# Kernel optimization log

Hardware: AMD Instinct MI355X
Metric: run time of the kernel (lower is better)

## Reference

```python
import jax, jax.numpy as jnp
import numpy as np

DIM = 1024
N_HEADS = 16
HEAD_DIM = DIM // N_HEADS
B, S = 2, 2048
NEG = -1e9  # additive causal mask value (finite, safe in low precision)


def setup_inputs() -> dict:
    key = jax.random.key(0)
    k_x, k_q, k_k, k_v, k_o = jax.random.split(key, 5)
    x = jax.random.normal(k_x, (B, S, DIM), dtype=jnp.float32)
    # causal additive mask, broadcastable to [B, H, S, S]
    causal = jnp.triu(jnp.ones((S, S), dtype=bool), k=1)
    mask = jnp.where(causal, NEG, 0.0).astype(jnp.float32)[None, None]
    scale = 1.0 / np.sqrt(DIM)
    wq = jax.random.normal(k_q, (DIM, DIM), dtype=jnp.float32) * scale
    wk = jax.random.normal(k_k, (DIM, DIM), dtype=jnp.float32) * scale
    wv = jax.random.normal(k_v, (DIM, DIM), dtype=jnp.float32) * scale
    wo = jax.random.normal(k_o, (DIM, DIM), dtype=jnp.float32) * scale
    return {"x": x, "mask": mask, "wq": wq, "wk": wk, "wv": wv, "wo": wo}


def reference(x, mask, wq, wk, wv, wo):
    bs, seqlen, _ = x.shape
    # nn.Linear(y) = y @ W^T ; weights stored as (out, in)
    q = (x @ wq.T).reshape(bs, seqlen, N_HEADS, HEAD_DIM)
    k = (x @ wk.T).reshape(bs, seqlen, N_HEADS, HEAD_DIM)
    v = (x @ wv.T).reshape(bs, seqlen, N_HEADS, HEAD_DIM)
    # scores: [B, H, S, S] — intentionally materialized, as in the original
    attn = jnp.einsum('bqhd,bkhd->bhqk', q, k) / np.sqrt(HEAD_DIM)
    attn = attn + mask
    attn = jax.nn.softmax(attn, axis=-1)
    out = jnp.einsum('bhqk,bkhd->bqhd', attn, v).reshape(bs, seqlen, DIM)
    return out @ wo.T
```

## Files before the change

### kernel.cpp

```cpp
#include <hip/hip_runtime.h>

typedef __attribute__((ext_vector_type(8))) short bf16x8;
typedef __attribute__((ext_vector_type(4))) float f32x4;
typedef __attribute__((ext_vector_type(16))) float f32x16;
typedef __attribute__((ext_vector_type(4))) unsigned short u16x4;
typedef __attribute__((ext_vector_type(8))) unsigned short u16x8;

#define DIM 1024
#define SEQ 2048
#define NHEAD 16
#define HDIM 64
#define C2 0.18033688011112042f

#define WAIT_VM4() asm volatile("s_waitcnt vmcnt(4)" ::: "memory")
#define WAIT_VM0() asm volatile("s_waitcnt vmcnt(0)" ::: "memory")
#define BAR() __builtin_amdgcn_s_barrier()
#define SCHEDB() __builtin_amdgcn_sched_barrier(0)

__device__ __forceinline__ unsigned short f2bf(float f) {
  union { float f; unsigned u; } v; v.f = f;
  unsigned r = v.u + 0x7fffu + ((v.u >> 16) & 1u);
  return (unsigned short)(r >> 16);
}

__device__ __forceinline__ float bf2f(unsigned short s) {
  union { unsigned u; float f; } v; v.u = ((unsigned)s) << 16;
  return v.f;
}

__device__ __forceinline__ void gload_lds16(const void* g, void* l) {
  __builtin_amdgcn_global_load_lds(
      (const __attribute__((address_space(1))) void*)g,
      (__attribute__((address_space(3))) void*)l, 16, 0, 0);
}

__device__ __forceinline__ f32x16 mfma32(bf16x8 a, bf16x8 b, f32x16 c) {
  return __builtin_amdgcn_mfma_f32_32x32x16_bf16(a, b, c, 0, 0, 0);
}

__device__ __forceinline__ unsigned cvtpk(float lo, float hi) {
  unsigned r;
  asm("v_cvt_pk_bf16_f32 %0, %1, %2" : "=v"(r) : "v"(lo), "v"(hi));
  return r;
}

__global__ void f2bf_all(const float* __restrict__ x, const float* __restrict__ wq,
                         const float* __restrict__ wk, const float* __restrict__ wv,
                         const float* __restrict__ wo, unsigned short* __restrict__ xb,
                         unsigned short* __restrict__ wb) {
  int blk = blockIdx.x;
  const float* src;
  unsigned short* dst;
  int rb;
  if (blk < 4096) { src = x; dst = xb; rb = blk; }
  else {
    int w = (blk - 4096) >> 10;
    src = w == 0 ? wq : w == 1 ? wk : w == 2 ? wv : wo;
    dst = wb + (size_t)w * 1048576;
    rb = (blk - 4096) & 1023;
  }
  int i = rb * 256 + threadIdx.x;
  float4 v = ((const float4*)src)[i];
  u16x4 o;
  o[0] = f2bf(v.x); o[1] = f2bf(v.y); o[2] = f2bf(v.z); o[3] = f2bf(v.w);
  ((u16x4*)dst)[i] = o;
}

__global__ __launch_bounds__(256) void gemm3(
    const unsigned short* __restrict__ xb,
    const unsigned short* __restrict__ wb,
    unsigned short* __restrict__ qkv) {
  __shared__ unsigned short As[2][4096];
  __shared__ unsigned short Bs[2][4096];
  const int bz = blockIdx.x;
  const unsigned short *A, *B;
  unsigned short* C;
  int m0, n0, ldc;
  float cscale = 1.0f;
  if (bz < 512) {
    int xcd = bz & 7, inner = bz >> 3;
    int mm = inner & 3, n = (inner >> 2) & 7, w = inner >> 5;
    m0 = (xcd * 4 + mm) * 128; n0 = n * 128;
    A = xb; B = wb + w * 1048576; C = qkv + w * 4194304; ldc = 1024;
    if (w == 0) cscale = C2;
  } else {
    int idx = bz - 512;
    int xcd = idx & 7, inner = idx >> 3;
    int tt = inner & 3, mv = inner >> 2;
    m0 = mv * 128; n0 = (xcd * 4 + tt) * 128;
    A = wb + 2 * 1048576; B = xb; C = qkv + 2 * 4194304; ldc = 4096;
  }
  const int tid = threadIdx.x;
  const int wv = tid >> 6, lane = tid & 63;
  const int g = lane >> 4, l16 = lane & 15;
  const int wm = (wv >> 1) * 64, wn = (wv & 1) * 64;
  const int sro = lane >> 2, sc4 = lane & 3;
  f32x4 acc[4][4] = {};

#define GSTAGE(IT, BUF)                                                        \
  {                                                                            \
    const int kt = (IT) * 32;                                                  \
    _Pragma("unroll")                                                          \
    for (int s = 0; s < 2; ++s) {                                              \
      int r = wv * 32 + s * 16 + sro;                                          \
      int cd = sc4 ^ ((r >> 1) & 3);                                           \
      gload_lds16(A + (long long)(m0 + r) * 1024 + kt + cd * 8,                \
                  &As[BUF][wv * 1024 + s * 512]);                              \
      gload_lds16(B + (long long)(n0 + r) * 1024 + kt + cd * 8,                \
                  &Bs[BUF][wv * 1024 + s * 512]);                              \
    }                                                                          \
  }

  GSTAGE(0, 0);
  GSTAGE(1, 1);

  for (int it = 0; it < 32; ++it) {
    const int buf = it & 1;
    WAIT_VM4();
    BAR();
    SCHEDB();
    bf16x8 af[4], bfr[4];
#pragma unroll
    for (int mf = 0; mf < 4; ++mf) {
      int row = wm + mf * 16 + l16;
      af[mf] = *(const bf16x8*)((const char*)&As[buf][0] + row * 64 +
                                ((g ^ ((row >> 1) & 3)) << 4));
    }
#pragma unroll
    for (int nf = 0; nf < 4; ++nf) {
      int row = wn + nf * 16 + l16;
      bfr[nf] = *(const bf16x8*)((const char*)&Bs[buf][0] + row * 64 +
                                 ((g ^ ((row >> 1) & 3)) << 4));
    }
#pragma unroll
    for (int mf = 0; mf < 4; ++mf)
#pragma unroll
      for (int nf = 0; nf < 4; ++nf)
        acc[mf][nf] = __builtin_amdgcn_mfma_f32_16x16x32_bf16(
            af[mf], bfr[nf], acc[mf][nf], 0, 0, 0);
    SCHEDB();
    BAR();
    if (it + 1 < 32) {
      int nx = (it + 2 < 32) ? it + 2 : 31;
      GSTAGE(nx, buf);
    }
  }

#pragma unroll
  for (int mf = 0; mf < 4; ++mf)
#pragma unroll
    for (int nf = 0; nf < 4; ++nf)
#pragma unroll
      for (int r = 0; r < 4; ++r) {
        long long m = m0 + wm + mf * 16 + g * 4 + r;
        long long n = n0 + wn + nf * 16 + l16;
        C[m * ldc + n] = f2bf(acc[mf][nf][r] * cscale);
      }
}

__global__ __launch_bounds__(256) void gemm_out(
    const unsigned short* __restrict__ A,
    const unsigned short* __restrict__ B,
    float* __restrict__ C) {
  __shared__ unsigned short As[2][4096];
  __shared__ unsigned short Bs[2][4096];
  const int tid = threadIdx.x;
  const int wv = tid >> 6, lane = tid & 63;
  const int g = lane >> 4, l16 = lane & 15;
  const int m0 = blockIdx.y * 128, n0 = blockIdx.x * 128;
  const int wm = (wv >> 1) * 64, wn = (wv & 1) * 64;
  const int sro = lane >> 2, sc4 = lane & 3;
  f32x4 acc[4][4] = {};

#define OSTAGE(IT, BUF)                                                        \
  {                                                                            \
    const int kt = (IT) * 32;                                                  \
    _Pragma("unroll")                                                          \
    for (int s = 0; s < 2; ++s) {                                              \
      int r = wv * 32 + s * 16 + sro;                                          \
      int cd = sc4 ^ ((r >> 1) & 3);                                           \
      gload_lds16(A + (long long)(m0 + r) * 1024 + kt + cd * 8,                \
                  &As[BUF][wv * 1024 + s * 512]);                              \
      gload_lds16(B + (long long)(n0 + r) * 1024 + kt + cd * 8,                \
                  &Bs[BUF][wv * 1024 + s * 512]);                              \
    }                                                                          \
  }

  OSTAGE(0, 0);
  OSTAGE(1, 1);

  for (int it = 0; it < 32; ++it) {
    const int buf = it & 1;
    WAIT_VM4();
    BAR();
    SCHEDB();
    bf16x8 af[4], bfr[4];
#pragma unroll
    for (int mf = 0; mf < 4; ++mf) {
      int row = wm + mf * 16 + l16;
      af[mf] = *(const bf16x8*)((const char*)&As[buf][0] + row * 64 +
                                ((g ^ ((row >> 1) & 3)) << 4));
    }
#pragma unroll
    for (int nf = 0; nf < 4; ++nf) {
      int row = wn + nf * 16 + l16;
      bfr[nf] = *(const bf16x8*)((const char*)&Bs[buf][0] + row * 64 +
                                 ((g ^ ((row >> 1) & 3)) << 4));
    }
#pragma unroll
    for (int mf = 0; mf < 4; ++mf)
#pragma unroll
      for (int nf = 0; nf < 4; ++nf)
        acc[mf][nf] = __builtin_amdgcn_mfma_f32_16x16x32_bf16(
            af[mf], bfr[nf], acc[mf][nf], 0, 0, 0);
    SCHEDB();
    BAR();
    if (it + 1 < 32) {
      int nx = (it + 2 < 32) ? it + 2 : 31;
      OSTAGE(nx, buf);
    }
  }

#pragma unroll
  for (int mf = 0; mf < 4; ++mf)
#pragma unroll
    for (int nf = 0; nf < 4; ++nf)
#pragma unroll
      for (int r = 0; r < 4; ++r) {
        long long m = m0 + wm + mf * 16 + g * 4 + r;
        long long n = n0 + wn + nf * 16 + l16;
        C[m * 1024 + n] = acc[mf][nf][r];
      }
}

__global__ __launch_bounds__(256, 4) void attn_kernel(
    const unsigned short* __restrict__ Qg,
    const unsigned short* __restrict__ Kg,
    const unsigned short* __restrict__ VTg,
    unsigned short* __restrict__ Og,
    unsigned short* __restrict__ pacc,
    float* __restrict__ pml) {
  __shared__ unsigned short Kls[2][4096];
  __shared__ unsigned short Vls[2][4096];

  const int tid = threadIdx.x;
  const int wv = tid >> 6, lane = tid & 63;
  const int l32 = lane & 31, hi = lane >> 5;
  const int h = blockIdx.y, b = blockIdx.z;

  const int i = blockIdx.x;
  int qt, c, cn;
  if (i < 16)      { qt = 15 - (i >> 2); c = i & 3; cn = 4; }
  else if (i < 28) { int j = i - 16; qt = 11 - j / 3; c = j % 3; cn = 3; }
  else if (i < 36) { int j = i - 28; qt = 7 - ((j >> 1)); c = j & 1; cn = 2; }
  else             { qt = 39 - i; c = 0; cn = 1; }

  const int nt = 2 * qt + 2;
  const int t0 = c * 8;
  const int tb = min(t0 + 8, nt);
  const int umax = 4 * qt + wv;

  const int q = qt * 128 + wv * 32 + l32;
  const long long bh = (long long)b * SEQ * DIM + h * HDIM;
  const long long vbase = (long long)h * HDIM * 4096 + b * SEQ;

  const unsigned short* Qrow = Qg + (long long)(b * SEQ + q) * DIM + h * HDIM;
  bf16x8 qf[4];
#pragma unroll
  for (int ds = 0; ds < 4; ++ds)
    qf[ds] = *(const bf16x8*)(Qrow + ds * 16 + hi * 8);
  WAIT_VM0();

  bf16x8 ones;
#pragma unroll
  for (int j = 0; j < 8; ++j) ones[j] = (short)0x3F80;

  f32x16 acc0 = {}, acc1 = {}, lacc = {};

  const int sr = lane >> 3, sc = lane & 7;
#define STAGE(T, BUF)                                                          \
  {                                                                            \
    const int kv0s = (T) * 64;                                                 \
    _Pragma("unroll")                                                          \
    for (int s = 0; s < 2; ++s) {                                              \
      int jj = wv * 2 + s;                                                     \
      int r = jj * 8 + sr;                                                     \
      int cs = (sc ^ (r & 7)) * 8;                                             \
      gload_lds16(Kg + bh + (long long)(kv0s + r) * DIM + cs,                  \
                  &Kls[BUF][jj * 512]);                                        \
      gload_lds16(VTg + vbase + (long long)r * 4096 + kv0s + cs,               \
                  &Vls[BUF][jj * 512]);                                        \
    }                                                                          \
  }

  STAGE(t0, 0);
  { int nx = (t0 + 1 < tb) ? t0 + 1 : tb - 1; STAGE(nx, 1); }

  for (int t = t0; t < tb; ++t) {
    const int buf = (t - t0) & 1;
    WAIT_VM4();
    BAR();
    SCHEDB();

#pragma unroll
    for (int s = 0; s < 2; ++s) {
      const int u = 2 * t + s;
      if (u <= umax) {
        f32x16 sv = {};
        __builtin_amdgcn_s_setprio(1);
#pragma unroll
        for (int ds = 0; ds < 4; ++ds) {
          const int cbk = (((ds << 1) | hi) ^ (l32 & 7)) * 16;
          bf16x8 kf = *(const bf16x8*)((const char*)&Kls[buf][0] +
                                       (s * 32 + l32) * 128 + cbk);
          sv = mfma32(kf, qf[ds], sv);
        }
        __builtin_amdgcn_s_setprio(0);

        if (u == umax) {
#pragma unroll
          for (int r = 0; r < 16; ++r) {
            int kw = (r & 3) + 8 * (r >> 2) + 4 * hi;
            if (kw > l32) sv[r] = -1e30f;
          }
        }

#pragma unroll
        for (int r = 0; r < 16; ++r) sv[r] = exp2f(sv[r]);

        __builtin_amdgcn_s_setprio(1);
#pragma unroll
        for (int kk = 0; kk < 2; ++kk) {
          const int base = kk * 8;
          unsigned a0 = cvtpk(sv[base + 0], sv[base + 1]);
          unsigned a1 = cvtpk(sv[base + 2], sv[base + 3]);
          unsigned a2 = cvtpk(sv[base + 4], sv[base + 5]);
          unsigned a3 = cvtpk(sv[base + 6], sv[base + 7]);
          asm("v_permlane32_swap_b32 %0, %1" : "+v"(a0), "+v"(a2));
          asm("v_permlane32_swap_b32 %0, %1" : "+v"(a1), "+v"(a3));
          union { unsigned u4[4]; bf16x8 v; } pf;
          pf.u4[0] = a0; pf.u4[1] = a1; pf.u4[2] = a2; pf.u4[3] = a3;
          const int slice = 2 * s + kk;
          const int cbv = (((slice << 1) | hi) ^ (l32 & 7)) * 16;
          bf16x8 v0 = *(const bf16x8*)((const char*)&Vls[buf][0] + l32 * 128 + cbv);
          bf16x8 v1 = *(const bf16x8*)((const char*)&Vls[buf][0] + (32 + l32) * 128 + cbv);
          acc0 = mfma32(v0, pf.v, acc0);
          acc1 = mfma32(v1, pf.v, acc1);
          lacc = mfma32(ones, pf.v, lacc);
        }
        __builtin_amdgcn_s_setprio(0);
      }
    }
    SCHEDB();
    BAR();
    if (t + 1 < tb) {
      int nx = (t + 2 < tb) ? t + 2 : tb - 1;
      STAGE(nx, buf);
    }
  }

  const float l_run = lacc[0];

  if (cn == 1) {
    const float inv_l = 1.0f / l_run;
    unsigned short* Orow = Og + (long long)(b * SEQ + q) * DIM + h * HDIM;
#pragma unroll
    for (int dblk = 0; dblk < 2; ++dblk) {
#pragma unroll
      for (int g4 = 0; g4 < 4; ++g4) {
        u16x4 o;
#pragma unroll
        for (int jv = 0; jv < 4; ++jv) {
          float v = (dblk ? acc1[g4 * 4 + jv] : acc0[g4 * 4 + jv]) * inv_l;
          o[jv] = f2bf(v);
        }
        *(u16x4*)(Orow + dblk * 32 + 8 * g4 + 4 * hi) = o;
      }
    }
  } else {
    const int sbase = qt < 8 ? 2 * (qt - 4) : qt < 12 ? 8 + 3 * (qt - 8) : 20 + 4 * (qt - 12);
    const int slot = (b * NHEAD + h) * 36 + sbase + c;
    unsigned short* pbase = pacc + (size_t)slot * 8192 + (wv * 32 + l32) * 64;
#pragma unroll
    for (int dblk = 0; dblk < 2; ++dblk) {
#pragma unroll
      for (int g4 = 0; g4 < 4; ++g4) {
        u16x4 o;
#pragma unroll
        for (int jv = 0; jv < 4; ++jv)
          o[jv] = f2bf(dblk ? acc1[g4 * 4 + jv] : acc0[g4 * 4 + jv]);
        *(u16x4*)(pbase + dblk * 32 + 8 * g4 + 4 * hi) = o;
      }
    }
    if (hi == 0) pml[slot * 128 + wv * 32 + l32] = l_run;
  }
}

__global__ __launch_bounds__(256) void attn_merge(
    const unsigned short* __restrict__ pacc,
    const float* __restrict__ pml,
    unsigned short* __restrict__ Og) {
  const int qt = 4 + blockIdx.x;
  const int h = blockIdx.y, b = blockIdx.z;
  const int cn = (qt >> 2) + 1;
  const int sbase = qt < 8 ? 2 * (qt - 4) : qt < 12 ? 8 + 3 * (qt - 8) : 20 + 4 * (qt - 12);
  const int base_slot = (b * NHEAD + h) * 36 + sbase;
  const int t = threadIdx.x;
  const int ql = t >> 1, d0 = (t & 1) * 32;

  float L = 0.f;
#pragma unroll
  for (int cc = 0; cc < 4; ++cc)
    if (cc < cn) L += pml[(base_slot + cc) * 128 + ql];
  const float invL = 1.0f / L;

  float o[32] = {};
#pragma unroll
  for (int cc = 0; cc < 4; ++cc)
    if (cc < cn) {
      const unsigned short* p = pacc + (size_t)(base_slot + cc) * 8192 + ql * 64 + d0;
#pragma unroll
      for (int k = 0; k < 32; k += 8) {
        u16x8 v = *(const u16x8*)(p + k);
#pragma unroll
        for (int jv = 0; jv < 8; ++jv) o[k + jv] += bf2f(v[jv]);
      }
    }

  const int q = qt * 128 + ql;
  unsigned short* orow = Og + (size_t)(b * SEQ + q) * DIM + h * HDIM + d0;
#pragma unroll
  for (int k = 0; k < 32; k += 8) {
    u16x8 ov;
#pragma unroll
    for (int jv = 0; jv < 8; ++jv) ov[jv] = f2bf(o[k + jv] * invL);
    *(u16x8*)(orow + k) = ov;
  }
}

extern "C" void kernel_launch(void* const* d_in, const int* in_sizes, int n_in,
                              void* d_out, int out_size, void* d_ws, size_t ws_size,
                              hipStream_t stream) {
  const float* x   = (const float*)d_in[0];
  const float* wq  = (const float*)d_in[2];
  const float* wk  = (const float*)d_in[3];
  const float* wv_ = (const float*)d_in[4];
  const float* wo  = (const float*)d_in[5];

  unsigned short* xb  = (unsigned short*)d_ws;
  unsigned short* wb  = xb + (size_t)4096 * 1024;
  unsigned short* qkv = wb + (size_t)4 * 1024 * 1024;
  unsigned short* ao  = qkv + (size_t)3 * 4096 * 1024;
  unsigned short* pacc = ao + (size_t)4096 * 1024;
  float* pml = (float*)(pacc + (size_t)1152 * 8192);

  f2bf_all<<<8192, 256, 0, stream>>>(x, wq, wk, wv_, wo, xb, wb);

  gemm3<<<768, 256, 0, stream>>>(xb, wb, qkv);

  attn_kernel<<<dim3(40, 16, 2), 256, 0, stream>>>(
      qkv, qkv + 4194304, qkv + 2 * 4194304, ao, pacc, pml);

  attn_merge<<<dim3(12, 16, 2), 256, 0, stream>>>(pacc, pml, ao);

  gemm_out<<<dim3(8, 32, 1), 256, 0, stream>>>(ao, wb + 3145728, (float*)d_out);
}
```

Measured before the change: 117.5 us.

## Drop LDS staging in attention; load K/V fragments directly from global

Replaces the double-buffered global-to-LDS staging of K and V tiles, along with its barriers, with per-wave direct global loads of K and V^T fragments into registers. K is register-prefetched one 32-key step ahead. The loop now runs per wave over its own key range, so waves no longer synchronise with each other. This removes LDS traffic and block barriers, but the four waves now each re-fetch the same K/V data from global/L2 with narrower, less coalesced accesses. It also swaps exp2f for the raw hardware exp2 intrinsic.

```diff
diff --git a/kernel.cpp b/kernel.cpp
--- a/kernel.cpp
+++ b/kernel.cpp
@@ -13,7 +13,6 @@
 #define C2 0.18033688011112042f
 
 #define WAIT_VM4() asm volatile("s_waitcnt vmcnt(4)" ::: "memory")
-#define WAIT_VM0() asm volatile("s_waitcnt vmcnt(0)" ::: "memory")
 #define BAR() __builtin_amdgcn_s_barrier()
 #define SCHEDB() __builtin_amdgcn_sched_barrier(0)
 
@@ -240,9 +239,6 @@
     unsigned short* __restrict__ Og,
     unsigned short* __restrict__ pacc,
     float* __restrict__ pml) {
-  __shared__ unsigned short Kls[2][4096];
-  __shared__ unsigned short Vls[2][4096];
-
   const int tid = threadIdx.x;
   const int wv = tid >> 6, lane = tid & 63;
   const int l32 = lane & 31, hi = lane >> 5;
@@ -255,10 +251,9 @@
   else if (i < 36) { int j = i - 28; qt = 7 - ((j >> 1)); c = j & 1; cn = 2; }
   else             { qt = 39 - i; c = 0; cn = 1; }
 
-  const int nt = 2 * qt + 2;
-  const int t0 = c * 8;
-  const int tb = min(t0 + 8, nt);
   const int umax = 4 * qt + wv;
+  const int u0 = c * 16;
+  const int uend = min(u0 + 16, umax + 1);
 
   const int q = qt * 128 + wv * 32 + l32;
   const long long bh = (long long)b * SEQ * DIM + h * HDIM;
@@ -269,7 +264,6 @@
 #pragma unroll
   for (int ds = 0; ds < 4; ++ds)
     qf[ds] = *(const bf16x8*)(Qrow + ds * 16 + hi * 8);
-  WAIT_VM0();
 
   bf16x8 ones;
 #pragma unroll
@@ -277,86 +271,69 @@
 
   f32x16 acc0 = {}, acc1 = {}, lacc = {};
 
-  const int sr = lane >> 3, sc = lane & 7;
-#define STAGE(T, BUF)                                                          \
-  {                                                                            \
-    const int kv0s = (T) * 64;                                                 \
-    _Pragma("unroll")                                                          \
-    for (int s = 0; s < 2; ++s) {                                              \
-      int jj = wv * 2 + s;                                                     \
-      int r = jj * 8 + sr;                                                     \
-      int cs = (sc ^ (r & 7)) * 8;                                             \
-      gload_lds16(Kg + bh + (long long)(kv0s + r) * DIM + cs,                  \
-                  &Kls[BUF][jj * 512]);                                        \
-      gload_lds16(VTg + vbase + (long long)r * 4096 + kv0s + cs,               \
-                  &Vls[BUF][jj * 512]);                                        \
-    }                                                                          \
-  }
-
-  STAGE(t0, 0);
-  { int nx = (t0 + 1 < tb) ? t0 + 1 : tb - 1; STAGE(nx, 1); }
-
-  for (int t = t0; t < tb; ++t) {
-    const int buf = (t - t0) & 1;
-    WAIT_VM4();
-    BAR();
-    SCHEDB();
-
-#pragma unroll
-    for (int s = 0; s < 2; ++s) {
-      const int u = 2 * t + s;
-      if (u <= umax) {
-        f32x16 sv = {};
-        __builtin_amdgcn_s_setprio(1);
-#pragma unroll
-        for (int ds = 0; ds < 4; ++ds) {
-          const int cbk = (((ds << 1) | hi) ^ (l32 & 7)) * 16;
-          bf16x8 kf = *(const bf16x8*)((const char*)&Kls[buf][0] +
-                                       (s * 32 + l32) * 128 + cbk);
-          sv = mfma32(kf, qf[ds], sv);
-        }
-        __builtin_amdgcn_s_setprio(0);
-
-        if (u == umax) {
-#pragma unroll
-          for (int r = 0; r < 16; ++r) {
-            int kw = (r & 3) + 8 * (r >> 2) + 4 * hi;
-            if (kw > l32) sv[r] = -1e30f;
-          }
-        }
-
-#pragma unroll
-        for (int r = 0; r < 16; ++r) sv[r] = exp2f(sv[r]);
-
-        __builtin_amdgcn_s_setprio(1);
-#pragma unroll
-        for (int kk = 0; kk < 2; ++kk) {
-          const int base = kk * 8;
-          unsigned a0 = cvtpk(sv[base + 0], sv[base + 1]);
-          unsigned a1 = cvtpk(sv[base + 2], sv[base + 3]);
-          unsigned a2 = cvtpk(sv[base + 4], sv[base + 5]);
-          unsigned a3 = cvtpk(sv[base + 6], sv[base + 7]);
-          asm("v_permlane32_swap_b32 %0, %1" : "+v"(a0), "+v"(a2));
-          asm("v_permlane32_swap_b32 %0, %1" : "+v"(a1), "+v"(a3));
-          union { unsigned u4[4]; bf16x8 v; } pf;
-          pf.u4[0] = a0; pf.u4[1] = a1; pf.u4[2] = a2; pf.u4[3] = a3;
-          const int slice = 2 * s + kk;
-          const int cbv = (((slice << 1) | hi) ^ (l32 & 7)) * 16;
-          bf16x8 v0 = *(const bf16x8*)((const char*)&Vls[buf][0] + l32 * 128 + cbv);
-          bf16x8 v1 = *(const bf16x8*)((const char*)&Vls[buf][0] + (32 + l32) * 128 + cbv);
-          acc0 = mfma32(v0, pf.v, acc0);
-          acc1 = mfma32(v1, pf.v, acc1);
-          lacc = mfma32(ones, pf.v, lacc);
-        }
-        __builtin_amdgcn_s_setprio(0);
-      }
-    }
-    SCHEDB();
-    BAR();
-    if (t + 1 < tb) {
-      int nx = (t + 2 < tb) ? t + 2 : tb - 1;
-      STAGE(nx, buf);
-    }
+  const unsigned short* Kbh = Kg + bh + hi * 8;
+  const unsigned short* Vbh = VTg + vbase + (long long)l32 * 4096 + hi * 8;
+
+  bf16x8 kf0, kf1, kf2, kf3;
+  if (u0 < uend) {
+    const unsigned short* kp = Kbh + (long long)(u0 * 32 + l32) * DIM;
+    kf0 = *(const bf16x8*)(kp);
+    kf1 = *(const bf16x8*)(kp + 16);
+    kf2 = *(const bf16x8*)(kp + 32);
+    kf3 = *(const bf16x8*)(kp + 48);
+  }
+
+  for (int u = u0; u < uend; ++u) {
+    f32x16 sv = {};
+    __builtin_amdgcn_s_setprio(1);
+    sv = mfma32(kf0, qf[0], sv);
+    sv = mfma32(kf1, qf[1], sv);
+    sv = mfma32(kf2, qf[2], sv);
+    sv = mfma32(kf3, qf[3], sv);
+    __builtin_amdgcn_s_setprio(0);
+
+    bf16x8 n0 = kf0, n1 = kf1, n2 = kf2, n3 = kf3;
+    if (u + 1 < uend) {
+      const unsigned short* kp = Kbh + (long long)((u + 1) * 32 + l32) * DIM;
+      n0 = *(const bf16x8*)(kp);
+      n1 = *(const bf16x8*)(kp + 16);
+      n2 = *(const bf16x8*)(kp + 32);
+      n3 = *(const bf16x8*)(kp + 48);
+    }
+
+    if (u == umax) {
+#pragma unroll
+      for (int r = 0; r < 16; ++r) {
+        int kw = (r & 3) + 8 * (r >> 2) + 4 * hi;
+        if (kw > l32) sv[r] = -1e30f;
+      }
+    }
+
+#pragma unroll
+    for (int r = 0; r < 16; ++r) sv[r] = __builtin_amdgcn_exp2f(sv[r]);
+
+    const unsigned short* vp = Vbh + u * 32;
+    __builtin_amdgcn_s_setprio(1);
+#pragma unroll
+    for (int kk = 0; kk < 2; ++kk) {
+      const int base = kk * 8;
+      unsigned a0 = cvtpk(sv[base + 0], sv[base + 1]);
+      unsigned a1 = cvtpk(sv[base + 2], sv[base + 3]);
+      unsigned a2 = cvtpk(sv[base + 4], sv[base + 5]);
+      unsigned a3 = cvtpk(sv[base + 6], sv[base + 7]);
+      asm("v_permlane32_swap_b32 %0, %1" : "+v"(a0), "+v"(a2));
+      asm("v_permlane32_swap_b32 %0, %1" : "+v"(a1), "+v"(a3));
+      union { unsigned u4[4]; bf16x8 v; } pf;
+      pf.u4[0] = a0; pf.u4[1] = a1; pf.u4[2] = a2; pf.u4[3] = a3;
+      bf16x8 v0 = *(const bf16x8*)(vp + kk * 16);
+      bf16x8 v1 = *(const bf16x8*)(vp + 32 * 4096 + kk * 16);
+      acc0 = mfma32(v0, pf.v, acc0);
+      acc1 = mfma32(v1, pf.v, acc1);
+      lacc = mfma32(ones, pf.v, lacc);
+    }
+    __builtin_amdgcn_s_setprio(0);
+
+    kf0 = n0; kf1 = n1; kf2 = n2; kf3 = n3;
   }
 
   const float l_run = lacc[0];
```

Result: slower. 169.5 us (+44.2%).
